# Performance work log

Hardware: AMD Instinct MI355X
Metric: run time of the kernel (lower is better)

The kernel has to match this reference:

```python
import jax, jax.numpy as jnp
import numpy as np

E = 1024      # embed_dim
H = 16        # num_heads
HD = E // H   # head_dim = 64
R = 8         # dora rank
T, B = 2048, 2


def setup_inputs() -> dict:
    key = jax.random.key(0)
    ks = jax.random.split(key, 16)
    query = jax.random.normal(ks[0], (T, B, E), dtype=jnp.float32)
    kk = jax.random.normal(ks[1], (T, B, E), dtype=jnp.float32)
    vv = jax.random.normal(ks[2], (T, B, E), dtype=jnp.float32)

    def make_dora(k1, k2, k3, k4):
        w = jax.random.normal(k1, (E, E), dtype=jnp.float32) * (E ** -0.5)
        m = jnp.linalg.norm(w)            # magnitude scalar (Frobenius norm)
        V = w / m                          # frozen direction, ||V||_F = 1
        A = jax.random.normal(k2, (R, E), dtype=jnp.float32) * (E ** -0.5)
        Bm = jax.random.normal(k3, (E, R), dtype=jnp.float32) * 0.01
        b = jax.random.normal(k4, (E,), dtype=jnp.float32) * 0.01
        return m, V, A, Bm, b

    mag_q, dir_q, A_q, B_q, bias_q = make_dora(ks[3], ks[4], ks[5], ks[6])
    mag_v, dir_v, A_v, B_v, bias_v = make_dora(ks[7], ks[8], ks[9], ks[10])
    k_w = jax.random.normal(ks[11], (E, E), dtype=jnp.float32) * (E ** -0.5)
    k_b = jax.random.normal(ks[12], (E,), dtype=jnp.float32) * 0.01
    out_w = jax.random.normal(ks[13], (E, E), dtype=jnp.float32) * (E ** -0.5)
    out_b = jax.random.normal(ks[14], (E,), dtype=jnp.float32) * 0.01
    return dict(query=query, key=kk, value=vv,
                mag_q=mag_q, dir_q=dir_q, A_q=A_q, B_q=B_q, bias_q=bias_q,
                mag_v=mag_v, dir_v=dir_v, A_v=A_v, B_v=B_v, bias_v=bias_v,
                k_w=k_w, k_b=k_b, out_w=out_w, out_b=out_b)


def _dora_linear(x, m, V, A, Bm, b):
    # W_eff = m * (V + B@A) / (||V + B@A||_F + 1e-8); out = x @ W_eff.T + b
    Vu = V + Bm @ A                      # [E, E]
    W = (m / (jnp.linalg.norm(Vu) + 1e-8)) * Vu
    return x @ W.T + b


def reference(query, key, value, mag_q, dir_q, A_q, B_q, bias_q,
              mag_v, dir_v, A_v, B_v, bias_v, k_w, k_b, out_w, out_b):
    # NOTE: source module ignores `key`/`value` and derives k, v from `query`.
    Tq, Bq, _ = query.shape
    q = _dora_linear(query, mag_q, dir_q, A_q, B_q, bias_q)   # [T, B, E]
    k = query @ k_w.T + k_b                                    # frozen K proj
    v = _dora_linear(query, mag_v, dir_v, A_v, B_v, bias_v)
    # (T, B, E) -> (B*H, T, HD), matching torch reshape/transpose
    q = q.reshape(Tq, Bq * H, HD).transpose(1, 0, 2)
    k = k.reshape(Tq, Bq * H, HD).transpose(1, 0, 2)
    v = v.reshape(Tq, Bq * H, HD).transpose(1, 0, 2)
    scale = HD ** -0.5
    attn = jnp.einsum('nqd,nkd->nqk', q, k) * scale            # [B*H, T, T]
    attn = jax.nn.softmax(attn, axis=-1)                       # dropout p=0
    out = jnp.einsum('nqk,nkd->nqd', attn, v)                  # [B*H, T, HD]
    out = out.transpose(1, 0, 2).reshape(Tq, Bq, E)
    out = out @ out_w.T + out_b
    return out
```

## Files before the change

### kernel.cpp

```cpp
#include <hip/hip_runtime.h>
#include <hip/hip_bf16.h>

#define E_DIM 1024
#define T_DIM 2048
#define B_DIM 2
#define H_DIM 16
#define HD_DIM 64
#define R_DIM 8
#define M_ROWS (T_DIM * B_DIM)
#define LOG2E 1.4426950408889634f

typedef __attribute__((ext_vector_type(8))) short bf16x8;
typedef __attribute__((ext_vector_type(4))) short bf16x4;
typedef __attribute__((ext_vector_type(4))) float f32x4;
typedef __attribute__((ext_vector_type(2))) unsigned uint2v;

#if __has_builtin(__builtin_amdgcn_exp2f)
#define EXP2F(x) __builtin_amdgcn_exp2f(x)
#else
#define EXP2F(x) exp2f(x)
#endif

__device__ __forceinline__ unsigned short f2bf(float f) {
  unsigned int u = __builtin_bit_cast(unsigned int, f);
  u += 0x7FFFu + ((u >> 16) & 1u);
  return (unsigned short)(u >> 16);
}

__device__ __forceinline__ unsigned cvt_pk_bf16(float lo, float hi) {
  unsigned r;
  asm("v_cvt_pk_bf16_f32 %0, %1, %2" : "=v"(r) : "v"(lo), "v"(hi));
  return r;
}

__device__ __forceinline__ f32x4 mfma16(bf16x4 a, bf16x4 b, f32x4 c) {
#if __has_builtin(__builtin_amdgcn_mfma_f32_16x16x16bf16_1k)
  return __builtin_amdgcn_mfma_f32_16x16x16bf16_1k(a, b, c, 0, 0, 0);
#elif __has_builtin(__builtin_amdgcn_mfma_f32_16x16x16_bf16)
  return __builtin_amdgcn_mfma_f32_16x16x16_bf16(a, b, c, 0, 0, 0);
#else
  asm("v_mfma_f32_16x16x16_bf16 %0, %1, %2, %0" : "+v"(c) : "v"(a), "v"(b));
  return c;
#endif
}

__device__ __forceinline__ void glds16(const unsigned short* g, unsigned short* l) {
  __builtin_amdgcn_global_load_lds(
      (__attribute__((address_space(1))) void*)(g),
      (__attribute__((address_space(3))) void*)(l), 16, 0, 0);
}

__global__ __launch_bounds__(256) void prep(
    const float* __restrict__ query, const float* __restrict__ k_w,
    const float* __restrict__ out_w,
    const float* __restrict__ dir_q, const float* __restrict__ A_q, const float* __restrict__ B_q,
    const float* __restrict__ dir_v, const float* __restrict__ A_v, const float* __restrict__ B_v,
    unsigned short* __restrict__ qA_bf, unsigned short* __restrict__ kw_bf,
    unsigned short* __restrict__ ow_bf,
    unsigned short* __restrict__ Wq, unsigned short* __restrict__ Wv,
    float* __restrict__ partials) {
  const int bid = blockIdx.x;
  if (bid < 6144) {
    int u = bid * 256 + threadIdx.x;
    const float* src;
    unsigned short* dst;
    if (u < 1048576) { src = query; dst = qA_bf; }
    else if (u < 1310720) { src = k_w; dst = kw_bf; u -= 1048576; }
    else { src = out_w; dst = ow_bf; u -= 1310720; }
    float4 f = reinterpret_cast<const float4*>(src)[u];
    ushort4 o;
    o.x = f2bf(f.x); o.y = f2bf(f.y); o.z = f2bf(f.z); o.w = f2bf(f.w);
    reinterpret_cast<ushort4*>(dst)[u] = o;
    return;
  }
  const int bid2 = bid - 6144;
  const int mat = bid2 >> 8, bx = bid2 & 255;
  const float* __restrict__ dir = mat ? dir_v : dir_q;
  const float* __restrict__ Am  = mat ? A_v   : A_q;
  const float* __restrict__ Bm  = mat ? B_v   : B_q;
  unsigned short* __restrict__ W = mat ? Wv : Wq;

  float sum = 0.0f;
  for (int idx = bx * 256 + threadIdx.x; idx < E_DIM * E_DIM; idx += 256 * 256) {
    int i = idx >> 10;
    int j = idx & (E_DIM - 1);
    float v = dir[idx];
#pragma unroll
    for (int r = 0; r < R_DIM; ++r)
      v += Bm[i * R_DIM + r] * Am[r * E_DIM + j];
    W[idx] = f2bf(v);
    sum += v * v;
  }
#pragma unroll
  for (int off = 32; off > 0; off >>= 1) sum += __shfl_down(sum, off);
  __shared__ float red[4];
  if ((threadIdx.x & 63) == 0) red[threadIdx.x >> 6] = sum;
  __syncthreads();
  if (threadIdx.x == 0)
    partials[mat * 256 + bx] = (red[0] + red[1]) + (red[2] + red[3]);
}

template <int OUT_MODE>
__device__ __forceinline__ void gemm_bt_core(
    const unsigned short* __restrict__ A, const unsigned short* __restrict__ W,
    const float* __restrict__ bias, float scale, float bscale,
    void* __restrict__ Cptr, int bm, int bn) {
  __shared__ unsigned short As[128 * 32];
  __shared__ unsigned short Bs[128 * 32];
  const int tid = threadIdx.x;
  const int w = tid >> 6, lane = tid & 63;
  const int lr = lane & 15, lg = lane >> 4;
  const int wm = w >> 1, wn = w & 1;

  f32x4 acc[4][4];
#pragma unroll
  for (int i = 0; i < 4; ++i)
#pragma unroll
    for (int j = 0; j < 4; ++j) acc[i][j] = (f32x4){0.f, 0.f, 0.f, 0.f};

  const int c0u = tid, c1u = 256 + tid;
  const int r0 = c0u >> 2, o0 = (c0u & 3) * 8;
  const int r1 = c1u >> 2, o1 = (c1u & 3) * 8;

  for (int k0 = 0; k0 < E_DIM; k0 += 32) {
    glds16(A + (size_t)(bm + r0) * E_DIM + k0 + o0, As + c0u * 8);
    glds16(W + (size_t)(bn + r0) * E_DIM + k0 + o0, Bs + c0u * 8);
    glds16(A + (size_t)(bm + r1) * E_DIM + k0 + o1, As + c1u * 8);
    glds16(W + (size_t)(bn + r1) * E_DIM + k0 + o1, Bs + c1u * 8);
    __syncthreads();

    bf16x8 af[4], bf[4];
#pragma unroll
    for (int i = 0; i < 4; ++i)
      af[i] = *reinterpret_cast<const bf16x8*>(As + (wm * 64 + i * 16 + lr) * 32 + lg * 8);
#pragma unroll
    for (int j = 0; j < 4; ++j)
      bf[j] = *reinterpret_cast<const bf16x8*>(Bs + (wn * 64 + j * 16 + lr) * 32 + lg * 8);
#pragma unroll
    for (int i = 0; i < 4; ++i)
#pragma unroll
      for (int j = 0; j < 4; ++j)
        acc[i][j] = __builtin_amdgcn_mfma_f32_16x16x32_bf16(af[i], bf[j], acc[i][j], 0, 0, 0);
    __syncthreads();
  }

  if (OUT_MODE == 2) {
#pragma unroll
    for (int i = 0; i < 4; ++i) {
      int rowbase = bm + wm * 64 + i * 16 + lg * 4;
      float4 bb = *reinterpret_cast<const float4*>(&bias[rowbase]);
      float bbv[4] = {bb.x, bb.y, bb.z, bb.w};
#pragma unroll
      for (int j = 0; j < 4; ++j) {
        int xrow = bn + wn * 64 + j * 16 + lr;
        int t = xrow >> 1, bsel = xrow & 1;
#pragma unroll
        for (int rr = 0; rr < 4; ++rr) {
          int wrow = rowbase + rr;
          float v = scale * acc[i][j][rr] + bbv[rr];
          int nn = (bsel << 4) | (wrow >> 6);
          int d = wrow & 63;
          reinterpret_cast<unsigned short*>(Cptr)[((size_t)nn * HD_DIM + d) * T_DIM + t] = f2bf(v);
        }
      }
    }
  } else {
#pragma unroll
    for (int i = 0; i < 4; ++i) {
      int row = bm + wm * 64 + i * 16 + lg * 4;
#pragma unroll
      for (int j = 0; j < 4; ++j) {
        int col = bn + wn * 64 + j * 16 + lr;
        float bv = bias[col] * bscale;
#pragma unroll
        for (int r = 0; r < 4; ++r) {
          float v = scale * acc[i][j][r] + bv;
          reinterpret_cast<unsigned short*>(Cptr)[(size_t)(row + r) * E_DIM + col] = f2bf(v);
        }
      }
    }
  }
}

__global__ __launch_bounds__(256, 2) void gemm_qkv(
    const unsigned short* __restrict__ Abf,
    const unsigned short* __restrict__ Wq, const unsigned short* __restrict__ Wk,
    const unsigned short* __restrict__ Wv,
    const float* __restrict__ bias_q, const float* __restrict__ k_b,
    const float* __restrict__ bias_v,
    const float* __restrict__ partials, const float* __restrict__ mag_q,
    const float* __restrict__ mag_v,
    unsigned short* __restrict__ qbuf, unsigned short* __restrict__ kbuf,
    unsigned short* __restrict__ vT) {
  const int bid = blockIdx.x;
  const int swz = (bid & 7) * 64 + (bid >> 3);
  const int tid = threadIdx.x;

  if (swz >= 256) {
    float s = partials[256 + tid];
#pragma unroll
    for (int off = 32; off > 0; off >>= 1) s += __shfl_down(s, off);
    __shared__ float redv[4];
    if ((tid & 63) == 0) redv[tid >> 6] = s;
    __syncthreads();
    float tot = (redv[0] + redv[1]) + (redv[2] + redv[3]);
    float scale = mag_v[0] / (sqrtf(tot) + 1e-8f);
    __syncthreads();
    const int idx = swz - 256;
    gemm_bt_core<2>(Wv, Abf, bias_v, scale, 1.0f, vT,
                    (idx >> 5) * 128, (idx & 31) * 128);
    return;
  }

  float s = partials[tid];
#pragma unroll
  for (int off = 32; off > 0; off >>= 1) s += __shfl_down(s, off);
  __shared__ float red[4];
  if ((tid & 63) == 0) red[tid >> 6] = s;
  __syncthreads();
  float tot = (red[0] + red[1]) + (red[2] + red[3]);
  const float sm = 0.125f * LOG2E;
  const float qscale = (mag_q[0] / (sqrtf(tot) + 1e-8f)) * sm;
  __syncthreads();

  const int bm = (swz >> 3) * 128, bn = (swz & 7) * 128;
  __shared__ unsigned short As[128 * 32];
  __shared__ unsigned short Bqs[128 * 32];
  __shared__ unsigned short Bks[128 * 32];
  const int w = tid >> 6, lane = tid & 63;
  const int lr = lane & 15, lg = lane >> 4;
  const int wm = w >> 1, wn = w & 1;

  f32x4 accq[4][4], acck[4][4];
#pragma unroll
  for (int i = 0; i < 4; ++i)
#pragma unroll
    for (int j = 0; j < 4; ++j) {
      accq[i][j] = (f32x4){0.f, 0.f, 0.f, 0.f};
      acck[i][j] = (f32x4){0.f, 0.f, 0.f, 0.f};
    }

  const int c0u = tid, c1u = 256 + tid;
  const int r0 = c0u >> 2, o0 = (c0u & 3) * 8;
  const int r1 = c1u >> 2, o1 = (c1u & 3) * 8;

  for (int k0 = 0; k0 < E_DIM; k0 += 32) {
    glds16(Abf + (size_t)(bm + r0) * E_DIM + k0 + o0, As + c0u * 8);
    glds16(Abf + (size_t)(bm + r1) * E_DIM + k0 + o1, As + c1u * 8);
    glds16(Wq + (size_t)(bn + r0) * E_DIM + k0 + o0, Bqs + c0u * 8);
    glds16(Wq + (size_t)(bn + r1) * E_DIM + k0 + o1, Bqs + c1u * 8);
    glds16(Wk + (size_t)(bn + r0) * E_DIM + k0 + o0, Bks + c0u * 8);
    glds16(Wk + (size_t)(bn + r1) * E_DIM + k0 + o1, Bks + c1u * 8);
    __syncthreads();

    bf16x8 af[4], bq[4], bk[4];
#pragma unroll
    for (int i = 0; i < 4; ++i)
      af[i] = *reinterpret_cast<const bf16x8*>(As + (wm * 64 + i * 16 + lr) * 32 + lg * 8);
#pragma unroll
    for (int j = 0; j < 4; ++j) {
      bq[j] = *reinterpret_cast<const bf16x8*>(Bqs + (wn * 64 + j * 16 + lr) * 32 + lg * 8);
      bk[j] = *reinterpret_cast<const bf16x8*>(Bks + (wn * 64 + j * 16 + lr) * 32 + lg * 8);
    }
#pragma unroll
    for (int i = 0; i < 4; ++i)
#pragma unroll
      for (int j = 0; j < 4; ++j) {
        accq[i][j] = __builtin_amdgcn_mfma_f32_16x16x32_bf16(af[i], bq[j], accq[i][j], 0, 0, 0);
        acck[i][j] = __builtin_amdgcn_mfma_f32_16x16x32_bf16(af[i], bk[j], acck[i][j], 0, 0, 0);
      }
    __syncthreads();
  }

#pragma unroll
  for (int i = 0; i < 4; ++i) {
    int row = bm + wm * 64 + i * 16 + lg * 4;
#pragma unroll
    for (int j = 0; j < 4; ++j) {
      int col = bn + wn * 64 + j * 16 + lr;
      float bq_ = bias_q[col] * sm;
      float bk_ = k_b[col];
#pragma unroll
      for (int r = 0; r < 4; ++r) {
        qbuf[(size_t)(row + r) * E_DIM + col] = f2bf(qscale * accq[i][j][r] + bq_);
        kbuf[(size_t)(row + r) * E_DIM + col] = f2bf(acck[i][j][r] + bk_);
      }
    }
  }
}

__global__ __launch_bounds__(256) void gemm_out(
    const unsigned short* __restrict__ Abf, const unsigned short* __restrict__ Wo,
    const float* __restrict__ bias, float* __restrict__ out) {
  const int bid = blockIdx.x;
  const int swz = (bid & 7) * 32 + (bid >> 3);
  const int bm = (swz >> 3) * 128, bn = (swz & 7) * 128;

  __shared__ unsigned short As[128 * 32];
  __shared__ unsigned short Bs[128 * 32];
  const int tid = threadIdx.x;
  const int w = tid >> 6, lane = tid & 63;
  const int lr = lane & 15, lg = lane >> 4;
  const int wm = w >> 1, wn = w & 1;

  f32x4 acc[4][4];
#pragma unroll
  for (int i = 0; i < 4; ++i)
#pragma unroll
    for (int j = 0; j < 4; ++j) acc[i][j] = (f32x4){0.f, 0.f, 0.f, 0.f};

  const int c0u = tid, c1u = 256 + tid;
  const int r0 = c0u >> 2, o0 = (c0u & 3) * 8;
  const int r1 = c1u >> 2, o1 = (c1u & 3) * 8;

  float4 ra0, ra1, rb0, rb1;
  ra0 = *reinterpret_cast<const float4*>(Abf + (size_t)(bm + r0) * E_DIM + o0);
  ra1 = *reinterpret_cast<const float4*>(Abf + (size_t)(bm + r1) * E_DIM + o1);
  rb0 = *reinterpret_cast<const float4*>(Wo + (size_t)(bn + r0) * E_DIM + o0);
  rb1 = *reinterpret_cast<const float4*>(Wo + (size_t)(bn + r1) * E_DIM + o1);

  for (int k0 = 0; k0 < E_DIM; k0 += 32) {
    __syncthreads();
    *reinterpret_cast<float4*>(As + c0u * 8) = ra0;
    *reinterpret_cast<float4*>(As + c1u * 8) = ra1;
    *reinterpret_cast<float4*>(Bs + c0u * 8) = rb0;
    *reinterpret_cast<float4*>(Bs + c1u * 8) = rb1;
    __syncthreads();
    if (k0 + 32 < E_DIM) {
      ra0 = *reinterpret_cast<const float4*>(Abf + (size_t)(bm + r0) * E_DIM + k0 + 32 + o0);
      ra1 = *reinterpret_cast<const float4*>(Abf + (size_t)(bm + r1) * E_DIM + k0 + 32 + o1);
      rb0 = *reinterpret_cast<const float4*>(Wo + (size_t)(bn + r0) * E_DIM + k0 + 32 + o0);
      rb1 = *reinterpret_cast<const float4*>(Wo + (size_t)(bn + r1) * E_DIM + k0 + 32 + o1);
    }

    bf16x8 af[4], bf[4];
#pragma unroll
    for (int i = 0; i < 4; ++i)
      af[i] = *reinterpret_cast<const bf16x8*>(As + (wm * 64 + i * 16 + lr) * 32 + lg * 8);
#pragma unroll
    for (int j = 0; j < 4; ++j)
      bf[j] = *reinterpret_cast<const bf16x8*>(Bs + (wn * 64 + j * 16 + lr) * 32 + lg * 8);
#pragma unroll
    for (int i = 0; i < 4; ++i)
#pragma unroll
      for (int j = 0; j < 4; ++j)
        acc[i][j] = __builtin_amdgcn_mfma_f32_16x16x32_bf16(af[i], bf[j], acc[i][j], 0, 0, 0);
  }

#pragma unroll
  for (int i = 0; i < 4; ++i) {
    int row = bm + wm * 64 + i * 16 + lg * 4;
#pragma unroll
    for (int j = 0; j < 4; ++j) {
      int col = bn + wn * 64 + j * 16 + lr;
      float bv = bias[col];
#pragma unroll
      for (int r = 0; r < 4; ++r)
        out[(size_t)(row + r) * E_DIM + col] = acc[i][j][r] + bv;
    }
  }
}

#define LDPK 72
#define LDPV 136

__global__ __launch_bounds__(512, 2) void attn_mfma(
    const unsigned short* __restrict__ qb, const unsigned short* __restrict__ kb,
    const unsigned short* __restrict__ vT, unsigned short* __restrict__ ob) {
  __shared__ unsigned short Ks2[128 * LDPK];
  __shared__ unsigned short Vt2[64 * LDPV];
  const int n = blockIdx.x, b = n >> 4, col0 = (n & 15) * HD_DIM;
  const int tid = threadIdx.x, w = tid >> 6, lane = tid & 63;
  const int lr = lane & 15, lg = lane >> 4;
  const int q0 = blockIdx.y * 256 + w * 32;

  bf16x8 qf[2][2];
#pragma unroll
  for (int rf = 0; rf < 2; ++rf)
#pragma unroll
    for (int ks = 0; ks < 2; ++ks)
      qf[rf][ks] = *reinterpret_cast<const bf16x8*>(
          qb + ((size_t)(q0 + rf * 16 + lr) * B_DIM + b) * E_DIM + col0 + ks * 32 + lg * 8);

  f32x4 accO[2][4];
#pragma unroll
  for (int rf = 0; rf < 2; ++rf)
#pragma unroll
    for (int df = 0; df < 4; ++df) accO[rf][df] = (f32x4){0.f, 0.f, 0.f, 0.f};
  float mrun0 = -1e30f, mrun1 = -1e30f, lrun0 = 0.f, lrun1 = 0.f;

  const int kr0 = tid >> 3, kc0 = (tid & 7) * 8;
  const int kr1 = 64 + kr0;
  const int vd0 = tid >> 4, vc0 = (tid & 15) * 8;
  const int vd1 = 32 + vd0;
  float4 rk0, rk1, rv0, rv1;
  rk0 = *reinterpret_cast<const float4*>(kb + ((size_t)kr0 * B_DIM + b) * E_DIM + col0 + kc0);
  rk1 = *reinterpret_cast<const float4*>(kb + ((size_t)kr1 * B_DIM + b) * E_DIM + col0 + kc0);
  rv0 = *reinterpret_cast<const float4*>(vT + ((size_t)n * HD_DIM + vd0) * T_DIM + vc0);
  rv1 = *reinterpret_cast<const float4*>(vT + ((size_t)n * HD_DIM + vd1) * T_DIM + vc0);

  for (int kt = 0; kt < T_DIM; kt += 128) {
    __syncthreads();
    *reinterpret_cast<float4*>(Ks2 + kr0 * LDPK + kc0) = rk0;
    *reinterpret_cast<float4*>(Ks2 + kr1 * LDPK + kc0) = rk1;
    *reinterpret_cast<float4*>(Vt2 + vd0 * LDPV + vc0) = rv0;
    *reinterpret_cast<float4*>(Vt2 + vd1 * LDPV + vc0) = rv1;
    __syncthreads();
    if (kt + 128 < T_DIM) {
      int kt2 = kt + 128;
      rk0 = *reinterpret_cast<const float4*>(kb + ((size_t)(kt2 + kr0) * B_DIM + b) * E_DIM + col0 + kc0);
      rk1 = *reinterpret_cast<const float4*>(kb + ((size_t)(kt2 + kr1) * B_DIM + b) * E_DIM + col0 + kc0);
      rv0 = *reinterpret_cast<const float4*>(vT + ((size_t)n * HD_DIM + vd0) * T_DIM + kt2 + vc0);
      rv1 = *reinterpret_cast<const float4*>(vT + ((size_t)n * HD_DIM + vd1) * T_DIM + kt2 + vc0);
    }

#pragma unroll
    for (int h = 0; h < 2; ++h) {
      const unsigned short* Kh = Ks2 + h * 64 * LDPK;
      const unsigned short* Vh = Vt2 + h * 64;

      f32x4 s[4][2];
#pragma unroll
      for (int kf = 0; kf < 4; ++kf)
#pragma unroll
        for (int rf = 0; rf < 2; ++rf) s[kf][rf] = (f32x4){0.f, 0.f, 0.f, 0.f};
      __builtin_amdgcn_s_setprio(1);
#pragma unroll
      for (int ks = 0; ks < 2; ++ks)
#pragma unroll
        for (int kf = 0; kf < 4; ++kf) {
          bf16x8 kfr = *reinterpret_cast<const bf16x8*>(Kh + (kf * 16 + lr) * LDPK + ks * 32 + lg * 8);
#pragma unroll
          for (int rf = 0; rf < 2; ++rf)
            s[kf][rf] = __builtin_amdgcn_mfma_f32_16x16x32_bf16(kfr, qf[rf][ks], s[kf][rf], 0, 0, 0);
        }
      __builtin_amdgcn_s_setprio(0);

      float pm0, pm1;
      {
        float a0 = fmaxf(fmaxf(s[0][0][0], s[0][0][1]), fmaxf(s[0][0][2], s[0][0][3]));
        float a1 = fmaxf(fmaxf(s[1][0][0], s[1][0][1]), fmaxf(s[1][0][2], s[1][0][3]));
        float a2 = fmaxf(fmaxf(s[2][0][0], s[2][0][1]), fmaxf(s[2][0][2], s[2][0][3]));
        float a3 = fmaxf(fmaxf(s[3][0][0], s[3][0][1]), fmaxf(s[3][0][2], s[3][0][3]));
        pm0 = fmaxf(fmaxf(a0, a1), fmaxf(a2, a3));
        float b0 = fmaxf(fmaxf(s[0][1][0], s[0][1][1]), fmaxf(s[0][1][2], s[0][1][3]));
        float b1 = fmaxf(fmaxf(s[1][1][0], s[1][1][1]), fmaxf(s[1][1][2], s[1][1][3]));
        float b2 = fmaxf(fmaxf(s[2][1][0], s[2][1][1]), fmaxf(s[2][1][2], s[2][1][3]));
        float b3 = fmaxf(fmaxf(s[3][1][0], s[3][1][1]), fmaxf(s[3][1][2], s[3][1][3]));
        pm1 = fmaxf(fmaxf(b0, b1), fmaxf(b2, b3));
      }
      pm0 = fmaxf(pm0, __shfl_xor(pm0, 16)); pm0 = fmaxf(pm0, __shfl_xor(pm0, 32));
      pm1 = fmaxf(pm1, __shfl_xor(pm1, 16)); pm1 = fmaxf(pm1, __shfl_xor(pm1, 32));

      const int resc = __any((pm0 > mrun0 + 8.0f) || (pm1 > mrun1 + 8.0f));
      float mn0 = mrun0, mn1 = mrun1;
      if (resc) { mn0 = fmaxf(mn0, pm0); mn1 = fmaxf(mn1, pm1); }

#pragma unroll
      for (int kf = 0; kf < 4; ++kf)
#pragma unroll
        for (int r = 0; r < 4; ++r) {
          s[kf][0][r] = EXP2F(s[kf][0][r] - mn0);
          s[kf][1][r] = EXP2F(s[kf][1][r] - mn1);
        }

      bf16x4 pa4[2][4];
#pragma unroll
      for (int rf = 0; rf < 2; ++rf)
#pragma unroll
        for (int kf = 0; kf < 4; ++kf) {
          uint2v u = (uint2v){cvt_pk_bf16(s[kf][rf][0], s[kf][rf][1]),
                              cvt_pk_bf16(s[kf][rf][2], s[kf][rf][3])};
          pa4[rf][kf] = __builtin_bit_cast(bf16x4, u);
        }

      f32x4 u0 = (s[0][0] + s[1][0]) + (s[2][0] + s[3][0]);
      f32x4 u1 = (s[0][1] + s[1][1]) + (s[2][1] + s[3][1]);
      float ps0 = (u0[0] + u0[1]) + (u0[2] + u0[3]);
      float ps1 = (u1[0] + u1[1]) + (u1[2] + u1[3]);
      ps0 += __shfl_xor(ps0, 16); ps0 += __shfl_xor(ps0, 32);
      ps1 += __shfl_xor(ps1, 16); ps1 += __shfl_xor(ps1, 32);

      if (resc) {
        float al0 = EXP2F(mrun0 - mn0), al1 = EXP2F(mrun1 - mn1);
        mrun0 = mn0; mrun1 = mn1;
        lrun0 = lrun0 * al0 + ps0; lrun1 = lrun1 * al1 + ps1;
#pragma unroll
        for (int r = 0; r < 4; ++r) {
          float a0 = __shfl(al0, (lg << 2) | r);
          float a1 = __shfl(al1, (lg << 2) | r);
#pragma unroll
          for (int df = 0; df < 4; ++df) { accO[0][df][r] *= a0; accO[1][df][r] *= a1; }
        }
      } else {
        lrun0 += ps0; lrun1 += ps1;
      }

      __builtin_amdgcn_s_setprio(1);
#pragma unroll
      for (int kf = 0; kf < 4; ++kf) {
#pragma unroll
        for (int df = 0; df < 4; ++df) {
          bf16x4 vf4 = *reinterpret_cast<const bf16x4*>(
              Vh + (df * 16 + lr) * LDPV + kf * 16 + lg * 4);
          accO[0][df] = mfma16(pa4[0][kf], vf4, accO[0][df]);
          accO[1][df] = mfma16(pa4[1][kf], vf4, accO[1][df]);
        }
      }
      __builtin_amdgcn_s_setprio(0);
    }
  }

#pragma unroll
  for (int rf = 0; rf < 2; ++rf)
#pragma unroll
    for (int r = 0; r < 4; ++r) {
      float lv = __shfl(rf ? lrun1 : lrun0, (lg << 2) | r);
      float inv = 1.0f / lv;
      int row = q0 + rf * 16 + lg * 4 + r;
      size_t base = ((size_t)row * B_DIM + b) * E_DIM + col0;
#pragma unroll
      for (int df = 0; df < 4; ++df)
        ob[base + df * 16 + lr] = f2bf(accO[rf][df][r] * inv);
    }
}

extern "C" void kernel_launch(void* const* d_in, const int* in_sizes, int n_in,
                              void* d_out, int out_size, void* d_ws, size_t ws_size,
                              hipStream_t stream) {
  const float* query  = (const float*)d_in[0];
  const float* mag_q  = (const float*)d_in[3];
  const float* dir_q  = (const float*)d_in[4];
  const float* A_q    = (const float*)d_in[5];
  const float* B_q    = (const float*)d_in[6];
  const float* bias_q = (const float*)d_in[7];
  const float* mag_v  = (const float*)d_in[8];
  const float* dir_v  = (const float*)d_in[9];
  const float* A_v    = (const float*)d_in[10];
  const float* B_v    = (const float*)d_in[11];
  const float* bias_v = (const float*)d_in[12];
  const float* k_w    = (const float*)d_in[13];
  const float* k_b    = (const float*)d_in[14];
  const float* out_w  = (const float*)d_in[15];
  const float* out_b  = (const float*)d_in[16];
  float* out = (float*)d_out;

  char* ws = (char*)d_ws;
  float* partials = (float*)ws;
  unsigned short* qA_bf = (unsigned short*)(ws + 4096);
  unsigned short* wq_bf = qA_bf + (size_t)M_ROWS * E_DIM;
  unsigned short* wv_bf = wq_bf + (size_t)E_DIM * E_DIM;
  unsigned short* kw_bf = wv_bf + (size_t)E_DIM * E_DIM;
  unsigned short* ow_bf = kw_bf + (size_t)E_DIM * E_DIM;
  unsigned short* qbuf  = ow_bf + (size_t)E_DIM * E_DIM;
  unsigned short* kbuf  = qbuf + (size_t)M_ROWS * E_DIM;
  unsigned short* vTbuf = kbuf + (size_t)M_ROWS * E_DIM;
  unsigned short* abuf  = vTbuf + (size_t)M_ROWS * E_DIM;

  prep<<<6656, 256, 0, stream>>>(query, k_w, out_w,
                                 dir_q, A_q, B_q, dir_v, A_v, B_v,
                                 qA_bf, kw_bf, ow_bf, wq_bf, wv_bf, partials);

  gemm_qkv<<<512, 256, 0, stream>>>(qA_bf, wq_bf, kw_bf, wv_bf,
                                    bias_q, k_b, bias_v,
                                    partials, mag_q, mag_v,
                                    qbuf, kbuf, vTbuf);
  attn_mfma<<<dim3(B_DIM * H_DIM, T_DIM / 256), 512, 0, stream>>>(
      qbuf, kbuf, vTbuf, abuf);
  gemm_out<<<256, 256, 0, stream>>>(abuf, ow_bf, out_b, out);
}
```

Measured before the change: 144.8 us.

## Widen V-projection tiles to 128x256 and double K-step in output GEMM

The V-projection blocks in the QKV kernel now compute a 128x256 tile (two B tiles sharing one A tile), which cuts those blocks from 256 to 128 and the grid from 512 to 384, matching the Q/K blocks' two-accumulator shape. The output GEMM now stages 64 K-elements per iteration through two LDS buffers, halving the number of barrier pairs. The intended gain is more operand reuse and fewer synchronisations; the cost is more registers and LDS per block, which may lower occupancy, and a less even wave count across CUs.

```diff
diff --git a/kernel.cpp b/kernel.cpp
--- a/kernel.cpp
+++ b/kernel.cpp
@@ -100,88 +100,6 @@
     partials[mat * 256 + bx] = (red[0] + red[1]) + (red[2] + red[3]);
 }
 
-template <int OUT_MODE>
-__device__ __forceinline__ void gemm_bt_core(
-    const unsigned short* __restrict__ A, const unsigned short* __restrict__ W,
-    const float* __restrict__ bias, float scale, float bscale,
-    void* __restrict__ Cptr, int bm, int bn) {
-  __shared__ unsigned short As[128 * 32];
-  __shared__ unsigned short Bs[128 * 32];
-  const int tid = threadIdx.x;
-  const int w = tid >> 6, lane = tid & 63;
-  const int lr = lane & 15, lg = lane >> 4;
-  const int wm = w >> 1, wn = w & 1;
-
-  f32x4 acc[4][4];
-#pragma unroll
-  for (int i = 0; i < 4; ++i)
-#pragma unroll
-    for (int j = 0; j < 4; ++j) acc[i][j] = (f32x4){0.f, 0.f, 0.f, 0.f};
-
-  const int c0u = tid, c1u = 256 + tid;
-  const int r0 = c0u >> 2, o0 = (c0u & 3) * 8;
-  const int r1 = c1u >> 2, o1 = (c1u & 3) * 8;
-
-  for (int k0 = 0; k0 < E_DIM; k0 += 32) {
-    glds16(A + (size_t)(bm + r0) * E_DIM + k0 + o0, As + c0u * 8);
-    glds16(W + (size_t)(bn + r0) * E_DIM + k0 + o0, Bs + c0u * 8);
-    glds16(A + (size_t)(bm + r1) * E_DIM + k0 + o1, As + c1u * 8);
-    glds16(W + (size_t)(bn + r1) * E_DIM + k0 + o1, Bs + c1u * 8);
-    __syncthreads();
-
-    bf16x8 af[4], bf[4];
-#pragma unroll
-    for (int i = 0; i < 4; ++i)
-      af[i] = *reinterpret_cast<const bf16x8*>(As + (wm * 64 + i * 16 + lr) * 32 + lg * 8);
-#pragma unroll
-    for (int j = 0; j < 4; ++j)
-      bf[j] = *reinterpret_cast<const bf16x8*>(Bs + (wn * 64 + j * 16 + lr) * 32 + lg * 8);
-#pragma unroll
-    for (int i = 0; i < 4; ++i)
-#pragma unroll
-      for (int j = 0; j < 4; ++j)
-        acc[i][j] = __builtin_amdgcn_mfma_f32_16x16x32_bf16(af[i], bf[j], acc[i][j], 0, 0, 0);
-    __syncthreads();
-  }
-
-  if (OUT_MODE == 2) {
-#pragma unroll
-    for (int i = 0; i < 4; ++i) {
-      int rowbase = bm + wm * 64 + i * 16 + lg * 4;
-      float4 bb = *reinterpret_cast<const float4*>(&bias[rowbase]);
-      float bbv[4] = {bb.x, bb.y, bb.z, bb.w};
-#pragma unroll
-      for (int j = 0; j < 4; ++j) {
-        int xrow = bn + wn * 64 + j * 16 + lr;
-        int t = xrow >> 1, bsel = xrow & 1;
-#pragma unroll
-        for (int rr = 0; rr < 4; ++rr) {
-          int wrow = rowbase + rr;
-          float v = scale * acc[i][j][rr] + bbv[rr];
-          int nn = (bsel << 4) | (wrow >> 6);
-          int d = wrow & 63;
-          reinterpret_cast<unsigned short*>(Cptr)[((size_t)nn * HD_DIM + d) * T_DIM + t] = f2bf(v);
-        }
-      }
-    }
-  } else {
-#pragma unroll
-    for (int i = 0; i < 4; ++i) {
-      int row = bm + wm * 64 + i * 16 + lg * 4;
-#pragma unroll
-      for (int j = 0; j < 4; ++j) {
-        int col = bn + wn * 64 + j * 16 + lr;
-        float bv = bias[col] * bscale;
-#pragma unroll
-        for (int r = 0; r < 4; ++r) {
-          float v = scale * acc[i][j][r] + bv;
-          reinterpret_cast<unsigned short*>(Cptr)[(size_t)(row + r) * E_DIM + col] = f2bf(v);
-        }
-      }
-    }
-  }
-}
-
 __global__ __launch_bounds__(256, 2) void gemm_qkv(
     const unsigned short* __restrict__ Abf,
     const unsigned short* __restrict__ Wq, const unsigned short* __restrict__ Wk,
@@ -193,8 +111,15 @@
     unsigned short* __restrict__ qbuf, unsigned short* __restrict__ kbuf,
     unsigned short* __restrict__ vT) {
   const int bid = blockIdx.x;
-  const int swz = (bid & 7) * 64 + (bid >> 3);
+  const int swz = (bid & 7) * 48 + (bid >> 3);
   const int tid = threadIdx.x;
+  const int w = tid >> 6, lane = tid & 63;
+  const int lr = lane & 15, lg = lane >> 4;
+  const int wm = w >> 1, wn = w & 1;
+
+  const int c0u = tid, c1u = 256 + tid;
+  const int r0 = c0u >> 2, o0 = (c0u & 3) * 8;
+  const int r1 = c1u >> 2, o1 = (c1u & 3) * 8;
 
   if (swz >= 256) {
     float s = partials[256 + tid];
@@ -204,11 +129,77 @@
     if ((tid & 63) == 0) redv[tid >> 6] = s;
     __syncthreads();
     float tot = (redv[0] + redv[1]) + (redv[2] + redv[3]);
-    float scale = mag_v[0] / (sqrtf(tot) + 1e-8f);
-    __syncthreads();
+    const float scale = mag_v[0] / (sqrtf(tot) + 1e-8f);
+    __syncthreads();
+
     const int idx = swz - 256;
-    gemm_bt_core<2>(Wv, Abf, bias_v, scale, 1.0f, vT,
-                    (idx >> 5) * 128, (idx & 31) * 128);
+    const int bmv = (idx >> 4) * 128;
+    const int bn0 = (idx & 15) * 256;
+
+    __shared__ unsigned short As[128 * 32];
+    __shared__ unsigned short B0s[128 * 32];
+    __shared__ unsigned short B1s[128 * 32];
+
+    f32x4 acc0[4][4], acc1[4][4];
+#pragma unroll
+    for (int i = 0; i < 4; ++i)
+#pragma unroll
+      for (int j = 0; j < 4; ++j) {
+        acc0[i][j] = (f32x4){0.f, 0.f, 0.f, 0.f};
+        acc1[i][j] = (f32x4){0.f, 0.f, 0.f, 0.f};
+      }
+
+    for (int k0 = 0; k0 < E_DIM; k0 += 32) {
+      glds16(Wv  + (size_t)(bmv + r0) * E_DIM + k0 + o0, As + c0u * 8);
+      glds16(Wv  + (size_t)(bmv + r1) * E_DIM + k0 + o1, As + c1u * 8);
+      glds16(Abf + (size_t)(bn0 + r0) * E_DIM + k0 + o0, B0s + c0u * 8);
+      glds16(Abf + (size_t)(bn0 + r1) * E_DIM + k0 + o1, B0s + c1u * 8);
+      glds16(Abf + (size_t)(bn0 + 128 + r0) * E_DIM + k0 + o0, B1s + c0u * 8);
+      glds16(Abf + (size_t)(bn0 + 128 + r1) * E_DIM + k0 + o1, B1s + c1u * 8);
+      __syncthreads();
+
+      bf16x8 af[4], b0[4], b1[4];
+#pragma unroll
+      for (int i = 0; i < 4; ++i)
+        af[i] = *reinterpret_cast<const bf16x8*>(As + (wm * 64 + i * 16 + lr) * 32 + lg * 8);
+#pragma unroll
+      for (int j = 0; j < 4; ++j) {
+        b0[j] = *reinterpret_cast<const bf16x8*>(B0s + (wn * 64 + j * 16 + lr) * 32 + lg * 8);
+        b1[j] = *reinterpret_cast<const bf16x8*>(B1s + (wn * 64 + j * 16 + lr) * 32 + lg * 8);
+      }
+#pragma unroll
+      for (int i = 0; i < 4; ++i)
+#pragma unroll
+        for (int j = 0; j < 4; ++j) {
+          acc0[i][j] = __builtin_amdgcn_mfma_f32_16x16x32_bf16(af[i], b0[j], acc0[i][j], 0, 0, 0);
+          acc1[i][j] = __builtin_amdgcn_mfma_f32_16x16x32_bf16(af[i], b1[j], acc1[i][j], 0, 0, 0);
+        }
+      __syncthreads();
+    }
+
+#pragma unroll
+    for (int p = 0; p < 2; ++p) {
+      const int bnp = bn0 + p * 128;
+#pragma unroll
+      for (int i = 0; i < 4; ++i) {
+        int rowbase = bmv + wm * 64 + i * 16 + lg * 4;
+        float4 bb = *reinterpret_cast<const float4*>(&bias_v[rowbase]);
+        float bbv[4] = {bb.x, bb.y, bb.z, bb.w};
+#pragma unroll
+        for (int j = 0; j < 4; ++j) {
+          int xrow = bnp + wn * 64 + j * 16 + lr;
+          int t = xrow >> 1, bsel = xrow & 1;
+#pragma unroll
+          for (int rr = 0; rr < 4; ++rr) {
+            int wrow = rowbase + rr;
+            float v = scale * (p ? acc1[i][j][rr] : acc0[i][j][rr]) + bbv[rr];
+            int nn = (bsel << 4) | (wrow >> 6);
+            int d = wrow & 63;
+            vT[((size_t)nn * HD_DIM + d) * T_DIM + t] = f2bf(v);
+          }
+        }
+      }
+    }
     return;
   }
 
@@ -227,9 +218,6 @@
   __shared__ unsigned short As[128 * 32];
   __shared__ unsigned short Bqs[128 * 32];
   __shared__ unsigned short Bks[128 * 32];
-  const int w = tid >> 6, lane = tid & 63;
-  const int lr = lane & 15, lg = lane >> 4;
-  const int wm = w >> 1, wn = w & 1;
 
   f32x4 accq[4][4], acck[4][4];
 #pragma unroll
@@ -239,10 +227,6 @@
       accq[i][j] = (f32x4){0.f, 0.f, 0.f, 0.f};
       acck[i][j] = (f32x4){0.f, 0.f, 0.f, 0.f};
     }
-
-  const int c0u = tid, c1u = 256 + tid;
-  const int r0 = c0u >> 2, o0 = (c0u & 3) * 8;
-  const int r1 = c1u >> 2, o1 = (c1u & 3) * 8;
 
   for (int k0 = 0; k0 < E_DIM; k0 += 32) {
     glds16(Abf + (size_t)(bm + r0) * E_DIM + k0 + o0, As + c0u * 8);
@@ -296,8 +280,8 @@
   const int swz = (bid & 7) * 32 + (bid >> 3);
   const int bm = (swz >> 3) * 128, bn = (swz & 7) * 128;
 
-  __shared__ unsigned short As[128 * 32];
-  __shared__ unsigned short Bs[128 * 32];
+  __shared__ unsigned short As[2][128 * 32];
+  __shared__ unsigned short Bs[2][128 * 32];
   const int tid = threadIdx.x;
   const int w = tid >> 6, lane = tid & 63;
   const int lr = lane & 15, lg = lane >> 4;
@@ -313,38 +297,52 @@
   const int r0 = c0u >> 2, o0 = (c0u & 3) * 8;
   const int r1 = c1u >> 2, o1 = (c1u & 3) * 8;
 
-  float4 ra0, ra1, rb0, rb1;
-  ra0 = *reinterpret_cast<const float4*>(Abf + (size_t)(bm + r0) * E_DIM + o0);
-  ra1 = *reinterpret_cast<const float4*>(Abf + (size_t)(bm + r1) * E_DIM + o1);
-  rb0 = *reinterpret_cast<const float4*>(Wo + (size_t)(bn + r0) * E_DIM + o0);
-  rb1 = *reinterpret_cast<const float4*>(Wo + (size_t)(bn + r1) * E_DIM + o1);
-
-  for (int k0 = 0; k0 < E_DIM; k0 += 32) {
-    __syncthreads();
-    *reinterpret_cast<float4*>(As + c0u * 8) = ra0;
-    *reinterpret_cast<float4*>(As + c1u * 8) = ra1;
-    *reinterpret_cast<float4*>(Bs + c0u * 8) = rb0;
-    *reinterpret_cast<float4*>(Bs + c1u * 8) = rb1;
-    __syncthreads();
-    if (k0 + 32 < E_DIM) {
-      ra0 = *reinterpret_cast<const float4*>(Abf + (size_t)(bm + r0) * E_DIM + k0 + 32 + o0);
-      ra1 = *reinterpret_cast<const float4*>(Abf + (size_t)(bm + r1) * E_DIM + k0 + 32 + o1);
-      rb0 = *reinterpret_cast<const float4*>(Wo + (size_t)(bn + r0) * E_DIM + k0 + 32 + o0);
-      rb1 = *reinterpret_cast<const float4*>(Wo + (size_t)(bn + r1) * E_DIM + k0 + 32 + o1);
-    }
-
-    bf16x8 af[4], bf[4];
-#pragma unroll
-    for (int i = 0; i < 4; ++i)
-      af[i] = *reinterpret_cast<const bf16x8*>(As + (wm * 64 + i * 16 + lr) * 32 + lg * 8);
-#pragma unroll
-    for (int j = 0; j < 4; ++j)
-      bf[j] = *reinterpret_cast<const bf16x8*>(Bs + (wn * 64 + j * 16 + lr) * 32 + lg * 8);
-#pragma unroll
-    for (int i = 0; i < 4; ++i)
+  float4 ra[2][2], rb[2][2];
+#pragma unroll
+  for (int h = 0; h < 2; ++h) {
+    int kk = h * 32;
+    ra[h][0] = *reinterpret_cast<const float4*>(Abf + (size_t)(bm + r0) * E_DIM + kk + o0);
+    ra[h][1] = *reinterpret_cast<const float4*>(Abf + (size_t)(bm + r1) * E_DIM + kk + o1);
+    rb[h][0] = *reinterpret_cast<const float4*>(Wo + (size_t)(bn + r0) * E_DIM + kk + o0);
+    rb[h][1] = *reinterpret_cast<const float4*>(Wo + (size_t)(bn + r1) * E_DIM + kk + o1);
+  }
+
+  for (int k0 = 0; k0 < E_DIM; k0 += 64) {
+    __syncthreads();
+#pragma unroll
+    for (int h = 0; h < 2; ++h) {
+      *reinterpret_cast<float4*>(As[h] + c0u * 8) = ra[h][0];
+      *reinterpret_cast<float4*>(As[h] + c1u * 8) = ra[h][1];
+      *reinterpret_cast<float4*>(Bs[h] + c0u * 8) = rb[h][0];
+      *reinterpret_cast<float4*>(Bs[h] + c1u * 8) = rb[h][1];
+    }
+    __syncthreads();
+    if (k0 + 64 < E_DIM) {
+#pragma unroll
+      for (int h = 0; h < 2; ++h) {
+        int kk = k0 + 64 + h * 32;
+        ra[h][0] = *reinterpret_cast<const float4*>(Abf + (size_t)(bm + r0) * E_DIM + kk + o0);
+        ra[h][1] = *reinterpret_cast<const float4*>(Abf + (size_t)(bm + r1) * E_DIM + kk + o1);
+        rb[h][0] = *reinterpret_cast<const float4*>(Wo + (size_t)(bn + r0) * E_DIM + kk + o0);
+        rb[h][1] = *reinterpret_cast<const float4*>(Wo + (size_t)(bn + r1) * E_DIM + kk + o1);
+      }
+    }
+
+#pragma unroll
+    for (int h = 0; h < 2; ++h) {
+      bf16x8 af[4], bf[4];
+#pragma unroll
+      for (int i = 0; i < 4; ++i)
+        af[i] = *reinterpret_cast<const bf16x8*>(As[h] + (wm * 64 + i * 16 + lr) * 32 + lg * 8);
 #pragma unroll
       for (int j = 0; j < 4; ++j)
-        acc[i][j] = __builtin_amdgcn_mfma_f32_16x16x32_bf16(af[i], bf[j], acc[i][j], 0, 0, 0);
+        bf[j] = *reinterpret_cast<const bf16x8*>(Bs[h] + (wn * 64 + j * 16 + lr) * 32 + lg * 8);
+#pragma unroll
+      for (int i = 0; i < 4; ++i)
+#pragma unroll
+        for (int j = 0; j < 4; ++j)
+          acc[i][j] = __builtin_amdgcn_mfma_f32_16x16x32_bf16(af[i], bf[j], acc[i][j], 0, 0, 0);
+    }
   }
 
 #pragma unroll
@@ -561,7 +559,7 @@
                                  dir_q, A_q, B_q, dir_v, A_v, B_v,
                                  qA_bf, kw_bf, ow_bf, wq_bf, wv_bf, partials);
 
-  gemm_qkv<<<512, 256, 0, stream>>>(qA_bf, wq_bf, kw_bf, wv_bf,
+  gemm_qkv<<<384, 256, 0, stream>>>(qA_bf, wq_bf, kw_bf, wv_bf,
                                     bias_q, k_b, bias_v,
                                     partials, mag_q, mag_v,
                                     qbuf, kbuf, vTbuf);
```

After: 172.3 us. 1.19x slower.
